# Performance work log

Hardware: AMD Instinct MI355X
Metric: run time of the kernel (lower is better)

## Reference

```python
import jax, jax.numpy as jnp
import numpy as np
from jax import lax

B, T, IN, S = 256, 256, 128, 1024


def _uniform(key, shape, fan_in):
    bound = 1.0 / np.sqrt(fan_in)
    return jax.random.uniform(key, shape, jnp.float32, -bound, bound)


def setup_inputs() -> dict:
    key = jax.random.key(0)
    ks = jax.random.split(key, 7)
    return {
        "x": jax.random.normal(ks[0], (B, T, IN), jnp.float32),
        "W_in": _uniform(ks[1], (S, IN), IN),
        "b_in": _uniform(ks[2], (S,), IN),
        "W_rec": _uniform(ks[3], (S, S), S),
        "b_rec": _uniform(ks[4], (S,), S),
        "W_rec2": _uniform(ks[5], (S, S), S),
        "b_rec2": _uniform(ks[6], (S,), S),
    }


def reference(x, W_in, b_in, W_rec, b_rec, W_rec2, b_rec2):
    bs, t_len = x.shape[0], x.shape[1]
    # Precompute the input projection for all timesteps in one GEMM: [B,T,S]
    ext = jnp.einsum("bti,si->bts", x, W_in) + b_in
    ext_t = jnp.swapaxes(ext, 0, 1)  # [T,B,S] for scan over time

    def step(state, e_t):
        s = jax.nn.relu((state + e_t) @ W_rec.T + b_rec)
        s = jax.nn.relu(s @ W_rec2.T + b_rec2)
        return s, None

    state0 = jnp.zeros((bs, W_rec.shape[0]), dtype=x.dtype)
    final_state, _ = lax.scan(step, state0, ext_t)
    # Original module copies the FINAL state into every timestep of out.
    out = jnp.broadcast_to(final_state[:, None, :], (bs, t_len, final_state.shape[-1]))
    return out
```

## Files before the change

### kernel.cpp

```cpp
#include <hip/hip_runtime.h>

typedef __attribute__((ext_vector_type(8))) short short8;
typedef __attribute__((ext_vector_type(4))) float float4_t;
typedef __attribute__((ext_vector_type(2))) float float2_t;
typedef __attribute__((ext_vector_type(4))) unsigned int uint4_t;
typedef unsigned short u16;
typedef unsigned int u32;
typedef unsigned long long u64;


__device__ __forceinline__ u16 f2bf(float f) {
  u32 u = __builtin_bit_cast(u32, f);
  u += 0x7fffu + ((u >> 16) & 1u);
  return (u16)(u >> 16);
}
__device__ __forceinline__ float bf2f(u16 h) {
  u32 u = ((u32)h) << 16;
  return __builtin_bit_cast(float, u);
}
__device__ __forceinline__ short8 cvt8(float4_t f0, float4_t f1) {
  short8 v;
  v[0]=(short)f2bf(f0[0]); v[1]=(short)f2bf(f0[1]); v[2]=(short)f2bf(f0[2]); v[3]=(short)f2bf(f0[3]);
  v[4]=(short)f2bf(f1[0]); v[5]=(short)f2bf(f1[1]); v[6]=(short)f2bf(f1[2]); v[7]=(short)f2bf(f1[3]);
  return v;
}

__global__ __launch_bounds__(256) void init_counter(u32* __restrict__ cnt) {
#pragma unroll
  for (int i = 0; i < 20; ++i) cnt[threadIdx.x + (i << 8)] = 0u;
}

__global__ __launch_bounds__(256) void prep_w(const float* __restrict__ Wr,
                                              const float* __restrict__ Wr2,
                                              u16* __restrict__ W1b,
                                              u16* __restrict__ W2b) {
  const int i = blockIdx.x * 256 + threadIdx.x;
  W1b[i] = f2bf(Wr[i]);
  W2b[i] = f2bf(Wr2[i]);
}

__global__ __launch_bounds__(256) void ext_gemm(const float* __restrict__ x,
                                                const float* __restrict__ Win,
                                                const float* __restrict__ bin,
                                                u16* __restrict__ ebuf) {
  const int wg = blockIdx.x;
  const int nt = wg & 15, mt = wg >> 4;
  const int tid = threadIdx.x;
  const int wave = tid >> 6, lane = tid & 63, quad = lane >> 4, lm = lane & 15;
  const int m0 = (mt << 6) + (wave << 4);
  const int n0 = nt << 6;

  short8 a[4];
#pragma unroll
  for (int ks = 0; ks < 4; ++ks) {
    const float* p = x + (m0 + lm) * 128 + (ks * 32 + quad * 8);
    a[ks] = cvt8(*(const float4_t*)p, *(const float4_t*)(p + 4));
  }
  short8 bfr[4][4];
#pragma unroll
  for (int nsub = 0; nsub < 4; ++nsub)
#pragma unroll
    for (int ks = 0; ks < 4; ++ks) {
      const float* p = Win + (n0 + (nsub << 4) + lm) * 128 + (ks * 32 + quad * 8);
      bfr[nsub][ks] = cvt8(*(const float4_t*)p, *(const float4_t*)(p + 4));
    }
  float4_t acc[4] = { {0,0,0,0},{0,0,0,0},{0,0,0,0},{0,0,0,0} };
#pragma unroll
  for (int ks = 0; ks < 4; ++ks)
#pragma unroll
    for (int nsub = 0; nsub < 4; ++nsub)
      acc[nsub] = __builtin_amdgcn_mfma_f32_16x16x32_bf16(a[ks], bfr[nsub][ks], acc[nsub], 0, 0, 0);

#pragma unroll
  for (int nsub = 0; nsub < 4; ++nsub) {
    const int n = n0 + (nsub << 4) + lm;
    const float bv = bin[n];
#pragma unroll
    for (int r = 0; r < 4; ++r) {
      const int m = m0 + (quad << 2) + r;
      const int b = m >> 8, t = m & 255;
      ebuf[(((t << 8) | b) << 10) + n] = f2bf(acc[nsub][r] + bv);
    }
  }
}

#define ALOAD8_SC1                                                           \
  asm volatile("global_load_dwordx4 %0, %8, off sc1\n\t"                     \
               "global_load_dwordx4 %1, %8, off offset:64 sc1\n\t"           \
               "global_load_dwordx4 %2, %8, off offset:128 sc1\n\t"          \
               "global_load_dwordx4 %3, %8, off offset:192 sc1\n\t"          \
               "global_load_dwordx4 %4, %8, off offset:256 sc1\n\t"          \
               "global_load_dwordx4 %5, %8, off offset:320 sc1\n\t"          \
               "global_load_dwordx4 %6, %8, off offset:384 sc1\n\t"          \
               "global_load_dwordx4 %7, %8, off offset:448 sc1\n\t"          \
               "s_waitcnt vmcnt(0)"                                          \
               : "=&v"(av[0]), "=&v"(av[1]), "=&v"(av[2]), "=&v"(av[3]),     \
                 "=&v"(av[4]), "=&v"(av[5]), "=&v"(av[6]), "=&v"(av[7])      \
               : "v"(rb) : "memory")

__global__ __launch_bounds__(512, 2) void rnn_persistent(
    const u16* __restrict__ ebuf, u16* __restrict__ buf0, u16* __restrict__ buf1,
    const u16* __restrict__ W1b, const u16* __restrict__ W2b,
    const float* __restrict__ b1, const float* __restrict__ b2,
    float* __restrict__ fbuf, u32* __restrict__ cnt) {
  __shared__ __align__(16) float Pt[4][16][68];
  __shared__ int s_fast;

  const int tid = threadIdx.x;
  const int wave = tid >> 6, lane = tid & 63, quad = lane >> 4, lm = lane & 15;
  const int mt = blockIdx.x & 15, ns = blockIdx.x >> 4;
  const int n0 = ns << 6;
  const int mat = wave >> 2, q = wave & 3;

  short8 wfrag[4][8];
  {
    const u16* Wm = mat ? W2b : W1b;
#pragma unroll
    for (int nsub = 0; nsub < 4; ++nsub)
#pragma unroll
      for (int ks = 0; ks < 8; ++ks)
        wfrag[nsub][ks] = __builtin_bit_cast(short8,
            *(const uint4*)(Wm + ((n0 + (nsub << 4) + lm) << 10) + (q << 8) + (ks << 5) + (quad << 3)));
  }

  const int me = tid >> 5;
  const int nc = (tid & 31) << 1;

  const float2_t bv1 = *(const float2_t*)(b1 + n0 + nc);
  const float2_t bv2 = *(const float2_t*)(b2 + n0 + nc);

  {
    const u32 xcc = (u32)__builtin_amdgcn_s_getreg(6164);
    u32* xcb = cnt + 4096;
    if (tid == 0) {
      __hip_atomic_store(xcb + blockIdx.x, xcc + 1u, __ATOMIC_RELAXED, __HIP_MEMORY_SCOPE_AGENT);
      asm volatile("s_waitcnt vmcnt(0)" ::: "memory");
      __hip_atomic_fetch_add(xcb + 256, 1u, __ATOMIC_RELAXED, __HIP_MEMORY_SCOPE_AGENT);
      while (__hip_atomic_load(xcb + 256, __ATOMIC_RELAXED, __HIP_MEMORY_SCOPE_AGENT) < 256u)
        __builtin_amdgcn_s_sleep(2);
    }
    __syncthreads();
    if (wave == 0) {
      bool ok = true;
      if (lane < 16) {
        u32 peer = __hip_atomic_load(xcb + mt + (lane << 4), __ATOMIC_RELAXED,
                                     __HIP_MEMORY_SCOPE_AGENT);
        ok = (peer == xcc + 1u);
      }
      int f = __all((int)ok) ? 1 : 0;
      if (lane == 0) s_fast = f;
    }
    __syncthreads();
  }
  const bool fast = (s_fast != 0);

  u32* gflags = cnt + (mt << 8);
  u32* myflag = gflags + (ns << 4);
  const u32* pollflag = gflags + (((q << 2) + (lane & 3)) << 4);

  for (int p = 0; p < 512; ++p) {
    const int t = p >> 1, st = p & 1;

    u32 e2 = 0;
    if (st && t < 255)
      e2 = *(const u32*)(ebuf + ((((t + 1) << 8) + (mt << 4) + me) << 10) + n0 + nc);

    const u16* uIn = st ? buf1 : (t == 0 ? ebuf : buf0);

    if (mat == st) {
      if (p) {
        int it = 0;
        while (true) {
          u32 v = __hip_atomic_load(pollflag, __ATOMIC_RELAXED, __HIP_MEMORY_SCOPE_AGENT);
          if (__all((int)(v >= (u32)p)) || ++it > 16384) break;
        }
        asm volatile("" ::: "memory");
      }
      short8 a8[8];
      const u16* rb = uIn + (((mt << 4) + lm) << 10) + (q << 8) + (quad << 3);
      {
        uint4_t av[8];
        ALOAD8_SC1;
#pragma unroll
        for (int ks = 0; ks < 8; ++ks) a8[ks] = __builtin_bit_cast(short8, av[ks]);
      }
      float4_t acc[4] = { {0,0,0,0},{0,0,0,0},{0,0,0,0},{0,0,0,0} };
#pragma unroll
      for (int ks = 0; ks < 8; ++ks) {
#pragma unroll
        for (int nsub = 0; nsub < 4; ++nsub)
          acc[nsub] = __builtin_amdgcn_mfma_f32_16x16x32_bf16(a8[ks], wfrag[nsub][ks], acc[nsub], 0, 0, 0);
      }
#pragma unroll
      for (int nsub = 0; nsub < 4; ++nsub)
#pragma unroll
        for (int r = 0; r < 4; ++r)
          Pt[q][(quad << 2) + r][(nsub << 4) + lm] = acc[nsub][r];
    }
    __syncthreads();

    {
      const float2_t p0 = *(const float2_t*)&Pt[0][me][nc];
      const float2_t p1 = *(const float2_t*)&Pt[1][me][nc];
      const float2_t p2 = *(const float2_t*)&Pt[2][me][nc];
      const float2_t p3 = *(const float2_t*)&Pt[3][me][nc];
      const float2_t bias = st ? bv2 : bv1;
      float2_t s = p0 + p1 + p2 + p3 + bias;
      s[0] = s[0] > 0.f ? s[0] : 0.f;
      s[1] = s[1] > 0.f ? s[1] : 0.f;
      const int gr = (mt << 4) + me;
      if (!st) {
        u32 o = (u32)f2bf(s[0]) | ((u32)f2bf(s[1]) << 16);
        u32* dst = (u32*)(buf1 + (gr << 10) + n0 + nc);
        if (fast) *dst = o;
        else __hip_atomic_store(dst, o, __ATOMIC_RELAXED, __HIP_MEMORY_SCOPE_AGENT);
      } else if (t < 255) {
        s[0] += bf2f((u16)(e2 & 0xffffu));
        s[1] += bf2f((u16)(e2 >> 16));
        u32 o = (u32)f2bf(s[0]) | ((u32)f2bf(s[1]) << 16);
        u32* dst = (u32*)(buf0 + (gr << 10) + n0 + nc);
        if (fast) *dst = o;
        else __hip_atomic_store(dst, o, __ATOMIC_RELAXED, __HIP_MEMORY_SCOPE_AGENT);
      } else {
        *(float2_t*)(fbuf + (gr << 10) + n0 + nc) = s;
      }
    }

    if (p < 511) {
      asm volatile("s_waitcnt vmcnt(0)" ::: "memory");
      __syncthreads();
      if (tid == 0) {
        if (fast) *myflag = (u32)(p + 1);
        else __hip_atomic_store(myflag, (u32)(p + 1), __ATOMIC_RELAXED, __HIP_MEMORY_SCOPE_AGENT);
      }
    }
  }
}

__global__ __launch_bounds__(256) void bcast(const float* __restrict__ fbuf,
                                             float* __restrict__ out) {
  const int idx4 = blockIdx.x * 256 + threadIdx.x;
  const int b = idx4 >> 16;
  const int s4 = idx4 & 255;
  const float4_t v = *(const float4_t*)(fbuf + (b << 10) + (s4 << 2));
  *(float4_t*)(out + ((size_t)idx4 << 2)) = v;
}

extern "C" void kernel_launch(void* const* d_in, const int* in_sizes, int n_in,
                              void* d_out, int out_size, void* d_ws, size_t ws_size,
                              hipStream_t stream) {
  const float* x     = (const float*)d_in[0];
  const float* Win   = (const float*)d_in[1];
  const float* bin   = (const float*)d_in[2];
  const float* Wrec  = (const float*)d_in[3];
  const float* brec  = (const float*)d_in[4];
  const float* Wrec2 = (const float*)d_in[5];
  const float* brec2 = (const float*)d_in[6];
  float* out = (float*)d_out;

  char* ws = (char*)d_ws;
  u16* W1b  = (u16*)(ws);
  u16* W2b  = (u16*)(ws + (2u << 20));
  u16* buf0 = (u16*)(ws + (4u << 20));
  u16* buf1 = (u16*)(ws + (4u << 20) + (512u << 10));
  float* fbuf = (float*)(ws + (5u << 20));
  u32* cnt  = (u32*)(ws + (6u << 20));
  u16* ebuf = (u16*)d_out;

  init_counter<<<1, 256, 0, stream>>>(cnt);
  prep_w<<<4096, 256, 0, stream>>>(Wrec, Wrec2, W1b, W2b);
  ext_gemm<<<16384, 256, 0, stream>>>(x, Win, bin, ebuf);

  void* args[] = { (void*)&ebuf, (void*)&buf0, (void*)&buf1, (void*)&W1b, (void*)&W2b,
                   (void*)&brec, (void*)&brec2, (void*)&fbuf, (void*)&cnt };
  (void)hipLaunchCooperativeKernel(reinterpret_cast<void*>(rnn_persistent),
                                   dim3(256), dim3(512), args, 0, stream);

  bcast<<<65536, 256, 0, stream>>>(fbuf, out);
}
```

Baseline: 1.563 ms.

## Drop per-step block barrier using per-wave flags and double-buffered partials

Each wave now publishes its own progress flag after its stores drain, and pollers check all 8 wave flags of each peer block, so the second __syncthreads per step is removed. The LDS partial-sum buffer is double-buffered by step parity so that skipping the barrier cannot overwrite data still being read. The next-timestep input prefetch is moved to the idle matrix's waves to hide its latency. In exchange there are more flag writes and wider polling, and correctness now depends on the per-wave flag protocol and on the parity buffering being enough to avoid LDS races.

Measured after the change: 1.579 ms. No clear change (+1.0%).

```diff
diff --git a/kernel.cpp b/kernel.cpp
--- a/kernel.cpp
+++ b/kernel.cpp
@@ -103,7 +103,7 @@
     const u16* __restrict__ W1b, const u16* __restrict__ W2b,
     const float* __restrict__ b1, const float* __restrict__ b2,
     float* __restrict__ fbuf, u32* __restrict__ cnt) {
-  __shared__ __align__(16) float Pt[4][16][68];
+  __shared__ __align__(16) float Pt[2][4][16][68];
   __shared__ int s_fast;
 
   const int tid = threadIdx.x;
@@ -155,19 +155,24 @@
   const bool fast = (s_fast != 0);
 
   u32* gflags = cnt + (mt << 8);
-  u32* myflag = gflags + (ns << 4);
-  const u32* pollflag = gflags + (((q << 2) + (lane & 3)) << 4);
+  u32* myflag = gflags + (ns << 4) + wave;
+  const u32* pollflag = gflags + (((q << 2) + ((lane >> 3) & 3)) << 4) + (lane & 7);
+
+  u32 e2v = 0;
 
   for (int p = 0; p < 512; ++p) {
     const int t = p >> 1, st = p & 1;
-
-    u32 e2 = 0;
-    if (st && t < 255)
-      e2 = *(const u32*)(ebuf + ((((t + 1) << 8) + (mt << 4) + me) << 10) + n0 + nc);
+    const bool active = (mat == st);
+
+    {
+      const int eidx = (p >> 1) + 1;
+      if (!active && eidx < 256)
+        e2v = *(const u32*)(ebuf + (((eidx << 8) + (mt << 4) + me) << 10) + n0 + nc);
+    }
 
     const u16* uIn = st ? buf1 : (t == 0 ? ebuf : buf0);
 
-    if (mat == st) {
+    if (active) {
       if (p) {
         int it = 0;
         while (true) {
@@ -195,15 +200,16 @@
       for (int nsub = 0; nsub < 4; ++nsub)
 #pragma unroll
         for (int r = 0; r < 4; ++r)
-          Pt[q][(quad << 2) + r][(nsub << 4) + lm] = acc[nsub][r];
+          Pt[p & 1][q][(quad << 2) + r][(nsub << 4) + lm] = acc[nsub][r];
     }
     __syncthreads();
 
     {
-      const float2_t p0 = *(const float2_t*)&Pt[0][me][nc];
-      const float2_t p1 = *(const float2_t*)&Pt[1][me][nc];
-      const float2_t p2 = *(const float2_t*)&Pt[2][me][nc];
-      const float2_t p3 = *(const float2_t*)&Pt[3][me][nc];
+      const int par = p & 1;
+      const float2_t p0 = *(const float2_t*)&Pt[par][0][me][nc];
+      const float2_t p1 = *(const float2_t*)&Pt[par][1][me][nc];
+      const float2_t p2 = *(const float2_t*)&Pt[par][2][me][nc];
+      const float2_t p3 = *(const float2_t*)&Pt[par][3][me][nc];
       const float2_t bias = st ? bv2 : bv1;
       float2_t s = p0 + p1 + p2 + p3 + bias;
       s[0] = s[0] > 0.f ? s[0] : 0.f;
@@ -215,8 +221,8 @@
         if (fast) *dst = o;
         else __hip_atomic_store(dst, o, __ATOMIC_RELAXED, __HIP_MEMORY_SCOPE_AGENT);
       } else if (t < 255) {
-        s[0] += bf2f((u16)(e2 & 0xffffu));
-        s[1] += bf2f((u16)(e2 >> 16));
+        s[0] += bf2f((u16)(e2v & 0xffffu));
+        s[1] += bf2f((u16)(e2v >> 16));
         u32 o = (u32)f2bf(s[0]) | ((u32)f2bf(s[1]) << 16);
         u32* dst = (u32*)(buf0 + (gr << 10) + n0 + nc);
         if (fast) *dst = o;
@@ -228,8 +234,7 @@
 
     if (p < 511) {
       asm volatile("s_waitcnt vmcnt(0)" ::: "memory");
-      __syncthreads();
-      if (tid == 0) {
+      if (lane == 0) {
         if (fast) *myflag = (u32)(p + 1);
         else __hip_atomic_store(myflag, (u32)(p + 1), __ATOMIC_RELAXED, __HIP_MEMORY_SCOPE_AGENT);
       }
```
